# Performance work log

Measured on AMD Instinct MI355X. Metric: run time of the kernel, lower is better.

## Reference

```python
import jax, jax.numpy as jnp
import numpy as np

N, D, K = 131072, 128, 512


def setup_inputs() -> dict:
    key = jax.random.key(0)
    k1, k2 = jax.random.split(key)
    inputs = jax.random.normal(k1, (N, D), dtype=jnp.float32)
    centroids = jax.random.normal(k2, (K, D), dtype=jnp.float32)
    return {"inputs": inputs, "centroids": centroids}


def reference(inputs, centroids):
    # distances[k, n] = sum_d (inputs[n, d] - centroids[k, d])^2
    x_sq = jnp.sum(inputs * inputs, axis=1)          # [N]
    c_sq = jnp.sum(centroids * centroids, axis=1)    # [K]
    cross = jnp.einsum('kd,nd->kn', centroids, inputs)  # [K, N]
    distances = c_sq[:, None] + x_sq[None, :] - 2.0 * cross  # [K, N]
    assignments = jnp.argmin(distances, axis=0)      # [N], int
    return distances, assignments
```

## Files before the change

kernel.cpp:

```cpp
#include <hip/hip_runtime.h>

#define N_PTS 131072
#define DIM   128
#define KC    512
#define NT    4
#define WAVES 4
#define BLOCK (WAVES * 64)
#define PTS_PER_WG (WAVES * NT * 16)
#define KTILES (KC / 16)
#define TILE_BYTES 8192
#define CHUNK 4
#define CHUNK_BYTES (CHUNK * TILE_BYTES)
#define NCHUNKS (KTILES / CHUNK)

typedef _Float16 half8 __attribute__((ext_vector_type(8)));
typedef float    f32x4 __attribute__((ext_vector_type(4)));

__global__ __launch_bounds__(128)
void prep_centroids(const float* __restrict__ c,
                    unsigned char* __restrict__ tiles,
                    float* __restrict__ csq) {
    const int k = blockIdx.x;
    const int d = threadIdx.x;
    float v = c[k * DIM + d];
    _Float16 hi = (_Float16)v;
    _Float16 lo = (_Float16)(v - (float)hi);

    const int kt = k >> 4, row = k & 15;
    const unsigned bsw = (unsigned)(2 * d) ^ (unsigned)((row & 7) << 4);
    unsigned char* tb = tiles + (size_t)kt * TILE_BYTES + row * 256 + bsw;
    *(_Float16*)(tb)        = hi;
    *(_Float16*)(tb + 4096) = lo;

    float s = v * v;
    #pragma unroll
    for (int off = 1; off < 64; off <<= 1) s += __shfl_xor(s, off);
    __shared__ float red[2];
    if ((d & 63) == 0) red[d >> 6] = s;
    __syncthreads();
    if (d == 0) csq[k] = red[0] + red[1];
}

__device__ __forceinline__ void stage16(const void* g, void* l) {
    __builtin_amdgcn_global_load_lds(
        (const __attribute__((address_space(1))) void*)g,
        (__attribute__((address_space(3))) void*)l, 16, 0, 0);
}

__device__ __forceinline__ void stage_tile(const unsigned char* src_tile,
                                           unsigned char* dst_tile, int lane) {
    #pragma unroll
    for (int j = 0; j < 8; ++j)
        stage16(src_tile + j * 1024 + lane * 16, dst_tile + j * 1024);
}

__global__ __launch_bounds__(BLOCK, 2)
void kmeans_mfma(const float* __restrict__ x,
                 const unsigned char* __restrict__ tiles,
                 const float* __restrict__ csq,
                 float* __restrict__ dist,
                 float* __restrict__ assign_out) {
    __shared__ alignas(16) unsigned char abuf[2 * CHUNK_BYTES];
    __shared__ alignas(16) float csq_lds[KC];

    const int tid  = threadIdx.x;
    const int wave = tid >> 6;
    const int lane = tid & 63;
    const int col  = lane & 15;
    const int g    = lane >> 4;
    const int n0   = blockIdx.x * PTS_PER_WG + wave * (NT * 16);

    stage_tile(tiles + (size_t)wave * TILE_BYTES,
               abuf + wave * TILE_BYTES, lane);

    csq_lds[tid]       = csq[tid];
    csq_lds[tid + 256] = csq[tid + 256];

    half8 bhi[NT][4], blo[NT][4];
    float xsq[NT];
    #pragma unroll
    for (int t = 0; t < NT; ++t) {
        const float* xp = x + (size_t)(n0 + t * 16 + col) * DIM;
        float s = 0.f;
        #pragma unroll
        for (int sb = 0; sb < 4; ++sb) {
            const int dbase = sb * 32 + g * 8;
            float4 v0 = *(const float4*)(xp + dbase);
            float4 v1 = *(const float4*)(xp + dbase + 4);
            float vv[8] = {v0.x, v0.y, v0.z, v0.w, v1.x, v1.y, v1.z, v1.w};
            half8 h, l;
            #pragma unroll
            for (int j = 0; j < 8; ++j) {
                _Float16 hh = (_Float16)vv[j];
                h[j] = hh;
                l[j] = (_Float16)(vv[j] - (float)hh);
                s = fmaf(vv[j], vv[j], s);
            }
            bhi[t][sb] = h;
            blo[t][sb] = l;
        }
        s += __shfl_xor(s, 16);
        s += __shfl_xor(s, 32);
        xsq[t] = s;
    }

    float bestd[NT];
    int   bestk[NT];
    #pragma unroll
    for (int t = 0; t < NT; ++t) { bestd[t] = INFINITY; bestk[t] = 0; }

    __syncthreads();

    int cur = 0;
    for (int c = 0; c < NCHUNKS; ++c) {
        if (c + 1 < NCHUNKS) {
            stage_tile(tiles + (size_t)((c + 1) * CHUNK + wave) * TILE_BYTES,
                       abuf + (cur ^ 1) * CHUNK_BYTES + wave * TILE_BYTES, lane);
        }
        __builtin_amdgcn_sched_barrier(0);

        #pragma unroll
        for (int i = 0; i < CHUNK; ++i) {
            const int kt = c * CHUNK + i;
            const unsigned char* buf = abuf + cur * CHUNK_BYTES + i * TILE_BYTES;

            half8 Ah[4], Al[4];
            #pragma unroll
            for (int sb = 0; sb < 4; ++sb) {
                const unsigned b = (unsigned)((sb * 64 + g * 16) ^ ((col & 7) << 4));
                Ah[sb] = *(const half8*)(buf + col * 256 + b);
                Al[sb] = *(const half8*)(buf + 4096 + col * 256 + b);
            }
            f32x4 cs4 = *(const f32x4*)(&csq_lds[kt * 16 + g * 4]);

            f32x4 acc[NT];
            #pragma unroll
            for (int t = 0; t < NT; ++t) {
                f32x4 a_ = {0.f, 0.f, 0.f, 0.f};
                #pragma unroll
                for (int sb = 0; sb < 4; ++sb) {
                    a_ = __builtin_amdgcn_mfma_f32_16x16x32_f16(Ah[sb], bhi[t][sb], a_, 0, 0, 0);
                    a_ = __builtin_amdgcn_mfma_f32_16x16x32_f16(Ah[sb], blo[t][sb], a_, 0, 0, 0);
                    a_ = __builtin_amdgcn_mfma_f32_16x16x32_f16(Al[sb], bhi[t][sb], a_, 0, 0, 0);
                }
                acc[t] = a_;
            }

            #pragma unroll
            for (int r = 0; r < 4; ++r) {
                const int kr = kt * 16 + g * 4 + r;
                float* drow = dist + (size_t)kr * N_PTS + n0 + col;
                #pragma unroll
                for (int t = 0; t < NT; ++t) {
                    float dv = fmaf(-2.f, acc[t][r], xsq[t] + cs4[r]);
                    drow[t * 16] = dv;
                    if (dv < bestd[t]) { bestd[t] = dv; bestk[t] = kr; }
                }
            }
        }

        if (c + 1 < NCHUNKS) {
            asm volatile("s_waitcnt vmcnt(63)" ::: "memory");
            __builtin_amdgcn_sched_barrier(0);
            __builtin_amdgcn_s_barrier();
            cur ^= 1;
        }
    }

    #pragma unroll
    for (int t = 0; t < NT; ++t) {
        float d = bestd[t];
        int   k = bestk[t];
        #pragma unroll
        for (int off = 16; off < 64; off <<= 1) {
            float od = __shfl_xor(d, off);
            int   ok = __shfl_xor(k, off);
            if (od < d || (od == d && ok < k)) { d = od; k = ok; }
        }
        if (g == 0) assign_out[n0 + t * 16 + col] = (float)k;
    }
}

extern "C" void kernel_launch(void* const* d_in, const int* in_sizes, int n_in,
                              void* d_out, int out_size, void* d_ws, size_t ws_size,
                              hipStream_t stream) {
    const float* x = (const float*)d_in[0];
    const float* c = (const float*)d_in[1];
    float* dist       = (float*)d_out;
    float* assign_out = dist + (size_t)KC * N_PTS;

    unsigned char* tiles = (unsigned char*)d_ws;
    float* csq = (float*)(tiles + (size_t)KTILES * TILE_BYTES);

    prep_centroids<<<KC, DIM, 0, stream>>>(c, tiles, csq);
    kmeans_mfma<<<N_PTS / PTS_PER_WG, BLOCK, 0, stream>>>(x, tiles, csq, dist, assign_out);
}
```

Before: 102.6 us.

## Replace double-buffered centroid staging with single larger buffer and rolled tile loop

Centroid tiles now load in chunks of eight tiles into a single LDS buffer instead of double-buffering four-tile chunks. Each chunk load sits between two barriers with full vmcnt waits, so prefetch no longer overlaps compute. The inner tile loop is no longer unrolled, which cuts code size and possibly register pressure. The trade is that every wave stalls on global-to-LDS loads at each chunk boundary, and the dist stores (which also count toward vmcnt) must drain before each wait.

```diff
diff --git a/kernel.cpp b/kernel.cpp
--- a/kernel.cpp
+++ b/kernel.cpp
@@ -9,7 +9,7 @@
 #define PTS_PER_WG (WAVES * NT * 16)
 #define KTILES (KC / 16)
 #define TILE_BYTES 8192
-#define CHUNK 4
+#define CHUNK 8
 #define CHUNK_BYTES (CHUNK * TILE_BYTES)
 #define NCHUNKS (KTILES / CHUNK)
 
@@ -47,11 +47,14 @@
         (__attribute__((address_space(3))) void*)l, 16, 0, 0);
 }
 
-__device__ __forceinline__ void stage_tile(const unsigned char* src_tile,
-                                           unsigned char* dst_tile, int lane) {
+__device__ __forceinline__ void stage_chunk(const unsigned char* src,
+                                            unsigned char* dst,
+                                            int wave, int lane) {
     #pragma unroll
-    for (int j = 0; j < 8; ++j)
-        stage16(src_tile + j * 1024 + lane * 16, dst_tile + j * 1024);
+    for (int j = 0; j < 16; ++j) {
+        const int off = wave * 16384 + j * 1024;
+        stage16(src + off + lane * 16, dst + off);
+    }
 }
 
 __global__ __launch_bounds__(BLOCK, 2)
@@ -60,7 +63,7 @@
                  const float* __restrict__ csq,
                  float* __restrict__ dist,
                  float* __restrict__ assign_out) {
-    __shared__ alignas(16) unsigned char abuf[2 * CHUNK_BYTES];
+    __shared__ alignas(16) unsigned char abuf[CHUNK_BYTES];
     __shared__ alignas(16) float csq_lds[KC];
 
     const int tid  = threadIdx.x;
@@ -70,8 +73,7 @@
     const int g    = lane >> 4;
     const int n0   = blockIdx.x * PTS_PER_WG + wave * (NT * 16);
 
-    stage_tile(tiles + (size_t)wave * TILE_BYTES,
-               abuf + wave * TILE_BYTES, lane);
+    stage_chunk(tiles, abuf, wave, lane);
 
     csq_lds[tid]       = csq[tid];
     csq_lds[tid + 256] = csq[tid + 256];
@@ -109,20 +111,22 @@
     #pragma unroll
     for (int t = 0; t < NT; ++t) { bestd[t] = INFINITY; bestk[t] = 0; }
 
+    asm volatile("s_waitcnt vmcnt(0)" ::: "memory");
     __syncthreads();
 
-    int cur = 0;
     for (int c = 0; c < NCHUNKS; ++c) {
-        if (c + 1 < NCHUNKS) {
-            stage_tile(tiles + (size_t)((c + 1) * CHUNK + wave) * TILE_BYTES,
-                       abuf + (cur ^ 1) * CHUNK_BYTES + wave * TILE_BYTES, lane);
+        if (c > 0) {
+            asm volatile("s_waitcnt lgkmcnt(0)" ::: "memory");
+            __builtin_amdgcn_s_barrier();
+            stage_chunk(tiles + (size_t)c * CHUNK_BYTES, abuf, wave, lane);
+            asm volatile("s_waitcnt vmcnt(0)" ::: "memory");
+            __builtin_amdgcn_s_barrier();
         }
-        __builtin_amdgcn_sched_barrier(0);
 
-        #pragma unroll
+        #pragma unroll 1
         for (int i = 0; i < CHUNK; ++i) {
             const int kt = c * CHUNK + i;
-            const unsigned char* buf = abuf + cur * CHUNK_BYTES + i * TILE_BYTES;
+            const unsigned char* buf = abuf + i * TILE_BYTES;
 
             half8 Ah[4], Al[4];
             #pragma unroll
@@ -158,13 +162,6 @@
                 }
             }
         }
-
-        if (c + 1 < NCHUNKS) {
-            asm volatile("s_waitcnt vmcnt(63)" ::: "memory");
-            __builtin_amdgcn_sched_barrier(0);
-            __builtin_amdgcn_s_barrier();
-            cur ^= 1;
-        }
     }
 
     #pragma unroll
```

Result: faster. 87.85 us (-14.4%).
